# Performance work log

Measured on AMD Instinct MI355X. Metric: run time of the kernel, lower is better.

Reference implementation:

```python
import jax, jax.numpy as jnp
import numpy as np

N_NODES = 100000


def gcn_conv(x, src, dst, norm, W, b, n_nodes):
    # PyG GCNConv: h = x @ W; out[i] = sum_{j->i} norm_ij * h[j]; out += b
    h = x @ W  # [N, F_out]
    msg = h[src] * norm[:, None]  # [E+N, F_out] gather + scale
    out = jax.ops.segment_sum(msg, dst, num_segments=n_nodes)
    return out + b


def setup_inputs() -> dict:
    key = jax.random.key(0)
    ks = jax.random.split(key, 5)
    n, e = N_NODES, 1600000
    d_in, d_h, d_out = 512, 128, 40
    x = jax.random.normal(ks[0], (n, d_in), dtype=jnp.float32)
    edge_index = jax.random.randint(ks[1], (2, e), 0, n, dtype=jnp.int64)
    # Glorot-ish scaled weights
    W1 = jax.random.normal(ks[2], (d_in, d_h), dtype=jnp.float32) * (1.0 / np.sqrt(d_in))
    b1 = jnp.zeros((d_h,), dtype=jnp.float32)
    W2 = jax.random.normal(ks[3], (d_h, d_out), dtype=jnp.float32) * (1.0 / np.sqrt(d_h))
    b2 = jnp.zeros((d_out,), dtype=jnp.float32)
    return {"x": x, "edge_index": edge_index, "W1": W1, "b1": b1, "W2": W2, "b2": b2}


def reference(x, edge_index, W1, b1, W2, b2):
    n = x.shape[0]
    # add self-loops (PyG default add_self_loops=True)
    loop = jnp.arange(n, dtype=edge_index.dtype)
    src = jnp.concatenate([edge_index[0], loop])
    dst = jnp.concatenate([edge_index[1], loop])
    # symmetric normalization: deg^-1/2[src] * deg^-1/2[dst]
    deg = jax.ops.segment_sum(jnp.ones_like(dst, dtype=x.dtype), dst, num_segments=n)
    dinv = jnp.where(deg > 0, jax.lax.rsqrt(jnp.maximum(deg, 1.0)), 0.0)
    norm = dinv[src] * dinv[dst]
    h = gcn_conv(x, src, dst, norm, W1, b1, n)
    h = jax.nn.relu(h)
    h = gcn_conv(h, src, dst, norm, W2, b2, n)
    return jax.nn.log_softmax(h, axis=1)
```

## Files before the change

kernel.cpp:

```cpp
#include <hip/hip_runtime.h>
#include <math.h>

#define NBSHIFT 7
#define CHUNK1 8192
#define CHUNK 2048
#define BCAP 4608

typedef __attribute__((ext_vector_type(8))) short short8;
typedef __attribute__((ext_vector_type(4))) float v4f;

__device__ __forceinline__ unsigned short f2bf(float f) {
    unsigned int u = __float_as_uint(f);
    u += 0x7FFFu + ((u >> 16) & 1u);
    return (unsigned short)(u >> 16);
}
__device__ __forceinline__ unsigned int packbf(float a, float b) {
    return (unsigned int)f2bf(a) | ((unsigned int)f2bf(b) << 16);
}
__device__ __forceinline__ void bf8_to_f32(uint4 v, float* f) {
    f[0] = __uint_as_float(v.x << 16); f[1] = __uint_as_float(v.x & 0xFFFF0000u);
    f[2] = __uint_as_float(v.y << 16); f[3] = __uint_as_float(v.y & 0xFFFF0000u);
    f[4] = __uint_as_float(v.z << 16); f[5] = __uint_as_float(v.z & 0xFFFF0000u);
    f[6] = __uint_as_float(v.w << 16); f[7] = __uint_as_float(v.w & 0xFFFF0000u);
}

__global__ __launch_bounds__(256) void binsize_kernel(const int* __restrict__ dst, int E,
                                                      int* __restrict__ binSizes, int nbins) {
    __shared__ int hist[1024];
    int tid = threadIdx.x;
    for (int i = tid; i < nbins; i += 256) hist[i] = 0;
    __syncthreads();
    int base = blockIdx.x * CHUNK1;
    int cnt = E - base; if (cnt > CHUNK1) cnt = CHUNK1;
    for (int i = tid; i < cnt; i += 256) atomicAdd(&hist[dst[base + i] >> NBSHIFT], 1);
    __syncthreads();
    for (int i = tid; i < nbins; i += 256)
        if (hist[i]) atomicAdd(&binSizes[i], hist[i]);
}

__global__ __launch_bounds__(256) void binscan_kernel(const int* __restrict__ binSizes,
                                                      int* __restrict__ bin_base,
                                                      int* __restrict__ bin_cursor,
                                                      int nbins, int E,
                                                      int* __restrict__ offsets, int N) {
    __shared__ int vals[1024];
    __shared__ int ws[256];
    int tid = threadIdx.x;
    for (int i = tid; i < 1024; i += 256) vals[i] = (i < nbins) ? binSizes[i] : 0;
    __syncthreads();
    int s0 = vals[4 * tid];
    int s1 = s0 + vals[4 * tid + 1];
    int s2 = s1 + vals[4 * tid + 2];
    int s3 = s2 + vals[4 * tid + 3];
    ws[tid] = s3;
    __syncthreads();
    for (int off = 1; off < 256; off <<= 1) {
        int v = (tid >= off) ? ws[tid - off] : 0;
        __syncthreads();
        ws[tid] += v;
        __syncthreads();
    }
    int add = (tid > 0) ? ws[tid - 1] : 0;
    int i0 = 4 * tid;
    int b0 = add, b1 = add + s0, b2 = add + s1, b3 = add + s2;
    if (i0     < nbins) { bin_base[i0]     = b0; bin_cursor[i0]     = b0; }
    if (i0 + 1 < nbins) { bin_base[i0 + 1] = b1; bin_cursor[i0 + 1] = b1; }
    if (i0 + 2 < nbins) { bin_base[i0 + 2] = b2; bin_cursor[i0 + 2] = b2; }
    if (i0 + 3 < nbins) { bin_base[i0 + 3] = b3; bin_cursor[i0 + 3] = b3; }
    if (tid == 0) { bin_base[nbins] = E; offsets[N] = E; }
}

__global__ __launch_bounds__(256) void binpass_kernel(const int* __restrict__ src,
                                                      const int* __restrict__ dst, int E,
                                                      int* __restrict__ bin_cursor,
                                                      unsigned int* __restrict__ bpairs, int nbins) {
    __shared__ unsigned int pk[CHUNK];
    __shared__ unsigned short binOf[CHUNK];
    __shared__ int hist[1024];
    __shared__ int scanned[1024];
    __shared__ int wsum[256];
    __shared__ int rank_[1024];
    __shared__ int gbase[1024];
    int tid = threadIdx.x;
    int base = blockIdx.x * CHUNK;
    int cnt = E - base; if (cnt > CHUNK) cnt = CHUNK;

    for (int i = tid; i < 1024; i += 256) { hist[i] = 0; rank_[i] = 0; }
    __syncthreads();
    for (int i = tid; i < cnt; i += 256)
        atomicAdd(&hist[dst[base + i] >> NBSHIFT], 1);
    __syncthreads();
    int s0 = hist[4 * tid];
    int s1 = s0 + hist[4 * tid + 1];
    int s2 = s1 + hist[4 * tid + 2];
    int s3 = s2 + hist[4 * tid + 3];
    wsum[tid] = s3;
    __syncthreads();
    for (int off = 1; off < 256; off <<= 1) {
        int v = (tid >= off) ? wsum[tid - off] : 0;
        __syncthreads();
        wsum[tid] += v;
        __syncthreads();
    }
    int add = (tid > 0) ? wsum[tid - 1] : 0;
    scanned[4 * tid]     = add + s0;
    scanned[4 * tid + 1] = add + s1;
    scanned[4 * tid + 2] = add + s2;
    scanned[4 * tid + 3] = add + s3;
    __syncthreads();
    for (int i = tid; i < cnt; i += 256) {
        int d = dst[base + i];
        int s = src[base + i];
        int b = d >> NBSHIFT;
        unsigned int p = (unsigned int)s | ((unsigned int)(d & 127) << 17);
        int r = atomicAdd(&rank_[b], 1);
        int pos = scanned[b] - hist[b] + r;
        pk[pos] = p;
        binOf[pos] = (unsigned short)b;
    }
    __syncthreads();
    for (int b = tid; b < nbins; b += 256)
        if (hist[b] > 0) gbase[b] = atomicAdd(&bin_cursor[b], hist[b]);
    __syncthreads();
    for (int i = tid; i < cnt; i += 256) {
        int b = binOf[i];
        int local = i - (scanned[b] - hist[b]);
        bpairs[gbase[b] + local] = pk[i];
    }
}

__global__ __launch_bounds__(256) void binsort_kernel(const unsigned int* __restrict__ bpairs,
                                                      const int* __restrict__ bin_base,
                                                      int* __restrict__ ssrc,
                                                      int* __restrict__ offsets,
                                                      float* __restrict__ dinv, int N) {
    __shared__ unsigned int pin[BCAP];
    __shared__ int pout[BCAP];
    __shared__ int hist[128];
    __shared__ int pref[128];
    __shared__ int rank_[128];
    int b = blockIdx.x, tid = threadIdx.x;
    int start = bin_base[b], end = bin_base[b + 1];
    int cnt = end - start;
    if (cnt > BCAP) cnt = BCAP;
    int n0 = b << NBSHIFT;
    if (tid < 128) { hist[tid] = 0; rank_[tid] = 0; }
    __syncthreads();
    for (int i = tid; i < cnt; i += 256) {
        unsigned int p = bpairs[start + i];
        pin[i] = p;
        atomicAdd(&hist[p >> 17], 1);
    }
    __syncthreads();
    if (tid < 128) pref[tid] = hist[tid];
    __syncthreads();
    for (int off = 1; off < 128; off <<= 1) {
        int v = 0;
        if (tid < 128 && tid >= off) v = pref[tid - off];
        __syncthreads();
        if (tid < 128) pref[tid] += v;
        __syncthreads();
    }
    int node = n0 + tid;
    if (tid < 128 && node < N) {
        offsets[node] = start + pref[tid] - hist[tid];
        dinv[node] = rsqrtf((float)(hist[tid] + 1));
    }
    __syncthreads();
    for (int i = tid; i < cnt; i += 256) {
        unsigned int p = pin[i];
        int d = p >> 17;
        int r = atomicAdd(&rank_[d], 1);
        pout[pref[d] - hist[d] + r] = (int)(p & 0x1FFFFu);
    }
    __syncthreads();
    for (int i = tid; i < cnt; i += 256) ssrc[start + i] = pout[i];
}

__global__ void w1cast_kernel(const float* __restrict__ W1, unsigned short* __restrict__ W1s) {
    int idx = blockIdx.x * 256 + threadIdx.x;
    int k = idx >> 7, n = idx & 127;
    int dstIdx = ((k >> 6) << 13) | (n << 6) | ((((k >> 3) & 7) ^ (n & 7)) << 3) | (k & 7);
    W1s[dstIdx] = f2bf(W1[idx]);
}

#define BM1 128
#define BK1 64

__global__ __launch_bounds__(256) void gemm1_mfma_kernel(const float* __restrict__ X,
                                                         const unsigned short* __restrict__ W1s,
                                                         unsigned short* __restrict__ H, int N) {
    __shared__ unsigned short SMEM[16384];
    unsigned short* As = SMEM;
    unsigned short* Bs = SMEM + 8192;
    int tid = threadIdx.x;
    int wave = tid >> 6, lane = tid & 63;
    int quad = lane >> 4, lr = lane & 15;
    int mBase = (wave & 1) * 64, nBase = (wave >> 1) * 64;
    int rowBase = blockIdx.x * BM1;

    v4f zero4 = {0.f, 0.f, 0.f, 0.f};
    v4f acc[4][4];
    #pragma unroll
    for (int i = 0; i < 4; i++)
        #pragma unroll
        for (int j = 0; j < 4; j++) acc[i][j] = zero4;

    float4 pfA0[4], pfA1[4];
    uint4  pfB[4];

    #define LOAD_A(K0)                                                                  \
        _Pragma("unroll")                                                               \
        for (int t = 0; t < 4; t++) {                                                   \
            int idx = tid + t * 256;                                                    \
            int r = idx >> 3, c = idx & 7;                                              \
            int gr = rowBase + r;                                                       \
            const float4* p = (const float4*)(X + (size_t)gr * 512 + (K0) + c * 8);     \
            bool ok = gr < N;                                                           \
            pfA0[t] = ok ? p[0] : make_float4(0.f, 0.f, 0.f, 0.f);                      \
            pfA1[t] = ok ? p[1] : make_float4(0.f, 0.f, 0.f, 0.f);                      \
        }
    #define LOAD_B(K0)                                                                  \
        _Pragma("unroll")                                                               \
        for (int t = 0; t < 4; t++)                                                     \
            pfB[t] = *(const uint4*)(W1s + (((K0) >> 6) << 13) + ((tid + t * 256) << 3));

    LOAD_A(0); LOAD_B(0);

    for (int k0 = 0; k0 < 512; k0 += BK1) {
        __syncthreads();
        #pragma unroll
        for (int t = 0; t < 4; t++) {
            int idx = tid + t * 256;
            int r = idx >> 3, c = idx & 7;
            uint4 v;
            v.x = packbf(pfA0[t].x, pfA0[t].y); v.y = packbf(pfA0[t].z, pfA0[t].w);
            v.z = packbf(pfA1[t].x, pfA1[t].y); v.w = packbf(pfA1[t].z, pfA1[t].w);
            *(uint4*)(&As[(r << 6) + ((c ^ (r & 7)) << 3)]) = v;
        }
        #pragma unroll
        for (int t = 0; t < 4; t++)
            *(uint4*)(&Bs[(tid + t * 256) << 3]) = pfB[t];
        __syncthreads();
        if (k0 + BK1 < 512) { LOAD_A(k0 + BK1); LOAD_B(k0 + BK1); }
        #pragma unroll
        for (int kc = 0; kc < BK1; kc += 32) {
            int cb = kc >> 3;
            short8 aF[4], bF[4];
            #pragma unroll
            for (int i = 0; i < 4; i++) {
                int m = mBase + i * 16 + lr;
                aF[i] = *(const short8*)(&As[m * 64 + (((cb + quad) ^ (m & 7)) << 3)]);
            }
            #pragma unroll
            for (int j = 0; j < 4; j++) {
                int n = nBase + j * 16 + lr;
                bF[j] = *(const short8*)(&Bs[n * 64 + (((cb + quad) ^ (n & 7)) << 3)]);
            }
            #pragma unroll
            for (int i = 0; i < 4; i++)
                #pragma unroll
                for (int j = 0; j < 4; j++)
                    acc[i][j] = __builtin_amdgcn_mfma_f32_16x16x32_bf16(aF[i], bF[j], acc[i][j], 0, 0, 0);
        }
    }
    __syncthreads();
    unsigned short* Cs = SMEM;
    #pragma unroll
    for (int i = 0; i < 4; i++) {
        #pragma unroll
        for (int r = 0; r < 4; r++) {
            int m = mBase + i * 16 + quad * 4 + r;
            #pragma unroll
            for (int j = 0; j < 4; j++)
                Cs[m * 128 + ((nBase + j * 16 + lr) ^ ((m & 7) << 4))] = f2bf(acc[i][j][r]);
        }
    }
    __syncthreads();
    #pragma unroll
    for (int t = 0; t < 8; t++) {
        int idx = tid + t * 256;
        int row = idx >> 4, c = idx & 15;
        int gr = rowBase + row;
        if (gr < N)
            *(uint4*)(H + (size_t)gr * 128 + c * 8) =
                *(const uint4*)(&Cs[row * 128 + ((c * 8) ^ ((row & 7) << 4))]);
    }
    #undef LOAD_A
    #undef LOAD_B
}

__global__ __launch_bounds__(256) void agg1_kernel(const unsigned short* __restrict__ h1,
                                                   const int* __restrict__ offsets,
                                                   const int* __restrict__ ssrc,
                                                   const float* __restrict__ dinv,
                                                   const float* __restrict__ bias,
                                                   unsigned short* __restrict__ a1, int N) {
    int lane = threadIdx.x & 15;
    int node = (blockIdx.x << 4) + (threadIdx.x >> 4);
    if (node >= N) return;
    const uint4* h = (const uint4*)h1;
    float di = dinv[node];
    float acc[8], t[8];
    bf8_to_f32(h[(size_t)node * 16 + lane], t);
    #pragma unroll
    for (int i = 0; i < 8; i++) acc[i] = di * t[i];
    int e = offsets[node], e1 = offsets[node + 1];
    for (; e + 3 < e1; e += 4) {
        int sA = ssrc[e], sB = ssrc[e + 1], sC = ssrc[e + 2], sD = ssrc[e + 3];
        float wA = dinv[sA], wB = dinv[sB], wC = dinv[sC], wD = dinv[sD];
        uint4 vA = h[(size_t)sA * 16 + lane];
        uint4 vB = h[(size_t)sB * 16 + lane];
        uint4 vC = h[(size_t)sC * 16 + lane];
        uint4 vD = h[(size_t)sD * 16 + lane];
        float fA[8], fB[8], fC[8], fD[8];
        bf8_to_f32(vA, fA); bf8_to_f32(vB, fB); bf8_to_f32(vC, fC); bf8_to_f32(vD, fD);
        #pragma unroll
        for (int i = 0; i < 8; i++) {
            acc[i] = fmaf(wA, fA[i], acc[i]);
            acc[i] = fmaf(wB, fB[i], acc[i]);
            acc[i] = fmaf(wC, fC[i], acc[i]);
            acc[i] = fmaf(wD, fD[i], acc[i]);
        }
    }
    for (; e < e1; e++) {
        int s = ssrc[e];
        float w = dinv[s];
        float fs[8];
        bf8_to_f32(h[(size_t)s * 16 + lane], fs);
        #pragma unroll
        for (int i = 0; i < 8; i++) acc[i] = fmaf(w, fs[i], acc[i]);
    }
    float4 b0 = ((const float4*)bias)[lane * 2];
    float4 b1v = ((const float4*)bias)[lane * 2 + 1];
    float bb[8] = {b0.x, b0.y, b0.z, b0.w, b1v.x, b1v.y, b1v.z, b1v.w};
    float o[8];
    #pragma unroll
    for (int i = 0; i < 8; i++) o[i] = fmaxf(fmaf(di, acc[i], bb[i]), 0.f);
    uint4 pv;
    pv.x = packbf(o[0], o[1]); pv.y = packbf(o[2], o[3]);
    pv.z = packbf(o[4], o[5]); pv.w = packbf(o[6], o[7]);
    ((uint4*)a1)[(size_t)node * 16 + lane] = pv;
}

__global__ __launch_bounds__(256) void gemm2_kernel(const unsigned short* __restrict__ A,
                                                    const float* __restrict__ W,
                                                    float* __restrict__ H, int N) {
    __shared__ float As2[128][64];
    __shared__ float Ws[128 * 40];
    int tid = threadIdx.x;
    int rowBase = blockIdx.x * 64;

    #pragma unroll
    for (int l = 0; l < 4; l++) {
        int e = tid + l * 256;
        int r = e >> 4;
        int kk = (e & 15) << 3;
        int grow = rowBase + r;
        float f[8] = {0.f, 0.f, 0.f, 0.f, 0.f, 0.f, 0.f, 0.f};
        if (grow < N) {
            uint4 v = *(const uint4*)(A + (size_t)grow * 128 + kk);
            bf8_to_f32(v, f);
        }
        #pragma unroll
        for (int q = 0; q < 8; q++) As2[kk + q][r] = f[q];
    }
    #pragma unroll
    for (int l = 0; l < 5; l++) {
        int e = tid + l * 256;
        *(float4*)&Ws[e << 2] = *(const float4*)&W[e << 2];
    }
    __syncthreads();

    int tx = tid & 7;
    int ty = tid >> 3;
    float acc[2][5];
    #pragma unroll
    for (int r = 0; r < 2; r++)
        #pragma unroll
        for (int c = 0; c < 5; c++) acc[r][c] = 0.f;

    #pragma unroll 8
    for (int k = 0; k < 128; k++) {
        float a0 = As2[k][ty * 2];
        float a1v = As2[k][ty * 2 + 1];
        #pragma unroll
        for (int c = 0; c < 5; c++) {
            float w = Ws[k * 40 + tx * 5 + c];
            acc[0][c] = fmaf(a0, w, acc[0][c]);
            acc[1][c] = fmaf(a1v, w, acc[1][c]);
        }
    }
    #pragma unroll
    for (int r = 0; r < 2; r++) {
        int grow = rowBase + ty * 2 + r;
        if (grow < N) {
            #pragma unroll
            for (int c = 0; c < 5; c++) H[grow * 40 + tx * 5 + c] = acc[r][c];
        }
    }
}

__global__ __launch_bounds__(256) void agg2_kernel(const float* __restrict__ h2,
                                                   const int* __restrict__ offsets,
                                                   const int* __restrict__ ssrc,
                                                   const float* __restrict__ dinv,
                                                   const float* __restrict__ bias,
                                                   float* __restrict__ out, int N) {
    int lane = threadIdx.x & 15;
    int node = (blockIdx.x << 4) + (threadIdx.x >> 4);
    if (node >= N) return;
    const float4* h = (const float4*)h2;
    float di = dinv[node];
    bool act = lane < 10;
    float a0 = 0.f, a1 = 0.f, a2 = 0.f, a3 = 0.f;
    if (act) {
        float4 v = h[(size_t)node * 10 + lane];
        a0 = di * v.x; a1 = di * v.y; a2 = di * v.z; a3 = di * v.w;
    }
    int e = offsets[node], e1 = offsets[node + 1];
    for (; e + 3 < e1; e += 4) {
        int sA = ssrc[e], sB = ssrc[e + 1], sC = ssrc[e + 2], sD = ssrc[e + 3];
        float wA = dinv[sA], wB = dinv[sB], wC = dinv[sC], wD = dinv[sD];
        if (act) {
            float4 vA = h[(size_t)sA * 10 + lane];
            float4 vB = h[(size_t)sB * 10 + lane];
            float4 vC = h[(size_t)sC * 10 + lane];
            float4 vD = h[(size_t)sD * 10 + lane];
            a0 = fmaf(wA, vA.x, a0); a1 = fmaf(wA, vA.y, a1);
            a2 = fmaf(wA, vA.z, a2); a3 = fmaf(wA, vA.w, a3);
            a0 = fmaf(wB, vB.x, a0); a1 = fmaf(wB, vB.y, a1);
            a2 = fmaf(wB, vB.z, a2); a3 = fmaf(wB, vB.w, a3);
            a0 = fmaf(wC, vC.x, a0); a1 = fmaf(wC, vC.y, a1);
            a2 = fmaf(wC, vC.z, a2); a3 = fmaf(wC, vC.w, a3);
            a0 = fmaf(wD, vD.x, a0); a1 = fmaf(wD, vD.y, a1);
            a2 = fmaf(wD, vD.z, a2); a3 = fmaf(wD, vD.w, a3);
        }
    }
    for (; e < e1; e++) {
        int s = ssrc[e];
        float w = dinv[s];
        if (act) {
            float4 v = h[(size_t)s * 10 + lane];
            a0 = fmaf(w, v.x, a0); a1 = fmaf(w, v.y, a1);
            a2 = fmaf(w, v.z, a2); a3 = fmaf(w, v.w, a3);
        }
    }
    float v0 = -INFINITY, v1 = -INFINITY, v2 = -INFINITY, v3 = -INFINITY;
    if (act) {
        float4 bb = ((const float4*)bias)[lane];
        v0 = fmaf(di, a0, bb.x); v1 = fmaf(di, a1, bb.y);
        v2 = fmaf(di, a2, bb.z); v3 = fmaf(di, a3, bb.w);
    }
    float m = fmaxf(fmaxf(v0, v1), fmaxf(v2, v3));
    #pragma unroll
    for (int off = 8; off; off >>= 1) m = fmaxf(m, __shfl_xor(m, off, 16));
    float s = act ? (expf(v0 - m) + expf(v1 - m) + expf(v2 - m) + expf(v3 - m)) : 0.f;
    #pragma unroll
    for (int off = 8; off; off >>= 1) s += __shfl_xor(s, off, 16);
    if (act) {
        float ls = logf(s);
        float4 o;
        o.x = v0 - m - ls; o.y = v1 - m - ls; o.z = v2 - m - ls; o.w = v3 - m - ls;
        ((float4*)out)[(size_t)node * 10 + lane] = o;
    }
}

extern "C" void kernel_launch(void* const* d_in, const int* in_sizes, int n_in,
                              void* d_out, int out_size, void* d_ws, size_t ws_size,
                              hipStream_t stream) {
    const float* x  = (const float*)d_in[0];
    const int*   ei = (const int*)d_in[1];
    const float* W1 = (const float*)d_in[2];
    const float* b1 = (const float*)d_in[3];
    const float* W2 = (const float*)d_in[4];
    const float* b2 = (const float*)d_in[5];
    float* out = (float*)d_out;

    int N = in_sizes[0] / 512;
    int E = in_sizes[1] / 2;
    const int* src = ei;
    const int* dst = ei + E;
    int nbins = (N + 127) >> NBSHIFT;

    char* ws = (char*)d_ws;
    size_t off = 0;
    auto alloc = [&](size_t bytes) -> void* {
        void* p = ws + off;
        off += (bytes + 255) & ~(size_t)255;
        return p;
    };
    int*   offsets   = (int*)alloc((size_t)(N + 1) * 4);
    float* dinv      = (float*)alloc((size_t)N * 4);
    int*   binSizes  = (int*)alloc((size_t)nbins * 4);
    int*   bin_base  = (int*)alloc((size_t)(nbins + 1) * 4);
    int*   bin_cur   = (int*)alloc((size_t)nbins * 4);
    int*   ssrc      = (int*)alloc((size_t)E * 4);
    unsigned short* W1s = (unsigned short*)alloc((size_t)128 * 512 * 2);
    unsigned short* h1  = (unsigned short*)alloc((size_t)N * 128 * 2);
    unsigned short* a1  = (unsigned short*)alloc((size_t)N * 128 * 2);
    float* h2        = (float*)alloc((size_t)N * 40 * 4);
    unsigned int* bpairs = (unsigned int*)h1;
    (void)ws_size; (void)n_in; (void)out_size;

    hipMemsetAsync(binSizes, 0, (size_t)nbins * 4, stream);
    binsize_kernel<<<(E + CHUNK1 - 1) / CHUNK1, 256, 0, stream>>>(dst, E, binSizes, nbins);
    binscan_kernel<<<1, 256, 0, stream>>>(binSizes, bin_base, bin_cur, nbins, E, offsets, N);
    binpass_kernel<<<(E + CHUNK - 1) / CHUNK, 256, 0, stream>>>(src, dst, E, bin_cur, bpairs, nbins);
    binsort_kernel<<<nbins, 256, 0, stream>>>(bpairs, bin_base, ssrc, offsets, dinv, N);
    w1cast_kernel<<<256, 256, 0, stream>>>(W1, W1s);
    gemm1_mfma_kernel<<<(N + BM1 - 1) / BM1, 256, 0, stream>>>(x, W1s, h1, N);
    agg1_kernel<<<(N + 15) / 16, 256, 0, stream>>>(h1, offsets, ssrc, dinv, b1, a1, N);
    gemm2_kernel<<<(N + 63) / 64, 256, 0, stream>>>(a1, W2, h2, N);
    agg2_kernel<<<(N + 15) / 16, 256, 0, stream>>>(h2, offsets, ssrc, dinv, b2, out, N);
}
```

Measured before the change: 537.4 us.

## Prescale GEMM outputs by dinv and widen bins to 256 nodes

Each layer's GEMM epilogue now multiplies its output row by the source node's deg^-1/2. The two aggregation kernels can then sum neighbour features directly, without a random dinv[src] load and a multiply for every edge. The CSR build also switches to 256-node bins with 8192-edge chunks in the bin pass, which reduces global atomics and the number of bins. The trade-off is fewer binpass blocks, more LDS per block, and a slightly different rounding order because values are scaled before the bf16 cast.

```diff
diff --git a/kernel.cpp b/kernel.cpp
--- a/kernel.cpp
+++ b/kernel.cpp
@@ -1,10 +1,10 @@
 #include <hip/hip_runtime.h>
 #include <math.h>
 
-#define NBSHIFT 7
+#define NBSHIFT 8
 #define CHUNK1 8192
-#define CHUNK 2048
-#define BCAP 4608
+#define CHUNK 8192
+#define BCAP 4864
 
 typedef __attribute__((ext_vector_type(8))) short short8;
 typedef __attribute__((ext_vector_type(4))) float v4f;
@@ -26,9 +26,9 @@
 
 __global__ __launch_bounds__(256) void binsize_kernel(const int* __restrict__ dst, int E,
                                                       int* __restrict__ binSizes, int nbins) {
-    __shared__ int hist[1024];
+    __shared__ int hist[512];
     int tid = threadIdx.x;
-    for (int i = tid; i < nbins; i += 256) hist[i] = 0;
+    for (int i = tid; i < 512; i += 256) hist[i] = 0;
     __syncthreads();
     int base = blockIdx.x * CHUNK1;
     int cnt = E - base; if (cnt > CHUNK1) cnt = CHUNK1;
@@ -43,16 +43,14 @@
                                                       int* __restrict__ bin_cursor,
                                                       int nbins, int E,
                                                       int* __restrict__ offsets, int N) {
-    __shared__ int vals[1024];
+    __shared__ int vals[512];
     __shared__ int ws[256];
     int tid = threadIdx.x;
-    for (int i = tid; i < 1024; i += 256) vals[i] = (i < nbins) ? binSizes[i] : 0;
-    __syncthreads();
-    int s0 = vals[4 * tid];
-    int s1 = s0 + vals[4 * tid + 1];
-    int s2 = s1 + vals[4 * tid + 2];
-    int s3 = s2 + vals[4 * tid + 3];
-    ws[tid] = s3;
+    for (int i = tid; i < 512; i += 256) vals[i] = (i < nbins) ? binSizes[i] : 0;
+    __syncthreads();
+    int s0 = vals[2 * tid];
+    int s1 = s0 + vals[2 * tid + 1];
+    ws[tid] = s1;
     __syncthreads();
     for (int off = 1; off < 256; off <<= 1) {
         int v = (tid >= off) ? ws[tid - off] : 0;
@@ -61,12 +59,9 @@
         __syncthreads();
     }
     int add = (tid > 0) ? ws[tid - 1] : 0;
-    int i0 = 4 * tid;
-    int b0 = add, b1 = add + s0, b2 = add + s1, b3 = add + s2;
-    if (i0     < nbins) { bin_base[i0]     = b0; bin_cursor[i0]     = b0; }
-    if (i0 + 1 < nbins) { bin_base[i0 + 1] = b1; bin_cursor[i0 + 1] = b1; }
-    if (i0 + 2 < nbins) { bin_base[i0 + 2] = b2; bin_cursor[i0 + 2] = b2; }
-    if (i0 + 3 < nbins) { bin_base[i0 + 3] = b3; bin_cursor[i0 + 3] = b3; }
+    int i0 = 2 * tid;
+    if (i0     < nbins) { bin_base[i0]     = add;      bin_cursor[i0]     = add; }
+    if (i0 + 1 < nbins) { bin_base[i0 + 1] = add + s0; bin_cursor[i0 + 1] = add + s0; }
     if (tid == 0) { bin_base[nbins] = E; offsets[N] = E; }
 }
 
@@ -76,43 +71,34 @@
                                                       unsigned int* __restrict__ bpairs, int nbins) {
     __shared__ unsigned int pk[CHUNK];
     __shared__ unsigned short binOf[CHUNK];
-    __shared__ int hist[1024];
-    __shared__ int scanned[1024];
-    __shared__ int wsum[256];
-    __shared__ int rank_[1024];
-    __shared__ int gbase[1024];
+    __shared__ int hist[512];
+    __shared__ int scanned[512];
+    __shared__ int rank_[512];
+    __shared__ int gbase[512];
     int tid = threadIdx.x;
     int base = blockIdx.x * CHUNK;
     int cnt = E - base; if (cnt > CHUNK) cnt = CHUNK;
 
-    for (int i = tid; i < 1024; i += 256) { hist[i] = 0; rank_[i] = 0; }
+    for (int i = tid; i < 512; i += 256) { hist[i] = 0; rank_[i] = 0; }
     __syncthreads();
     for (int i = tid; i < cnt; i += 256)
         atomicAdd(&hist[dst[base + i] >> NBSHIFT], 1);
     __syncthreads();
-    int s0 = hist[4 * tid];
-    int s1 = s0 + hist[4 * tid + 1];
-    int s2 = s1 + hist[4 * tid + 2];
-    int s3 = s2 + hist[4 * tid + 3];
-    wsum[tid] = s3;
-    __syncthreads();
-    for (int off = 1; off < 256; off <<= 1) {
-        int v = (tid >= off) ? wsum[tid - off] : 0;
-        __syncthreads();
-        wsum[tid] += v;
-        __syncthreads();
-    }
-    int add = (tid > 0) ? wsum[tid - 1] : 0;
-    scanned[4 * tid]     = add + s0;
-    scanned[4 * tid + 1] = add + s1;
-    scanned[4 * tid + 2] = add + s2;
-    scanned[4 * tid + 3] = add + s3;
-    __syncthreads();
+    scanned[tid] = hist[tid]; scanned[tid + 256] = hist[tid + 256];
+    __syncthreads();
+    for (int off = 1; off < 512; off <<= 1) {
+        int i0 = tid, i1 = tid + 256;
+        int v0 = (i0 >= off) ? scanned[i0 - off] : 0;
+        int v1 = (i1 >= off) ? scanned[i1 - off] : 0;
+        __syncthreads();
+        scanned[i0] += v0; scanned[i1] += v1;
+        __syncthreads();
+    }
     for (int i = tid; i < cnt; i += 256) {
         int d = dst[base + i];
         int s = src[base + i];
         int b = d >> NBSHIFT;
-        unsigned int p = (unsigned int)s | ((unsigned int)(d & 127) << 17);
+        unsigned int p = (unsigned int)s | ((unsigned int)(d & 255) << 17);
         int r = atomicAdd(&rank_[b], 1);
         int pos = scanned[b] - hist[b] + r;
         pk[pos] = p;
@@ -136,15 +122,15 @@
                                                       float* __restrict__ dinv, int N) {
     __shared__ unsigned int pin[BCAP];
     __shared__ int pout[BCAP];
-    __shared__ int hist[128];
-    __shared__ int pref[128];
-    __shared__ int rank_[128];
+    __shared__ int hist[256];
+    __shared__ int pref[256];
+    __shared__ int rank_[256];
     int b = blockIdx.x, tid = threadIdx.x;
     int start = bin_base[b], end = bin_base[b + 1];
     int cnt = end - start;
     if (cnt > BCAP) cnt = BCAP;
     int n0 = b << NBSHIFT;
-    if (tid < 128) { hist[tid] = 0; rank_[tid] = 0; }
+    hist[tid] = 0; rank_[tid] = 0;
     __syncthreads();
     for (int i = tid; i < cnt; i += 256) {
         unsigned int p = bpairs[start + i];
@@ -152,17 +138,16 @@
         atomicAdd(&hist[p >> 17], 1);
     }
     __syncthreads();
-    if (tid < 128) pref[tid] = hist[tid];
-    __syncthreads();
-    for (int off = 1; off < 128; off <<= 1) {
-        int v = 0;
-        if (tid < 128 && tid >= off) v = pref[tid - off];
-        __syncthreads();
-        if (tid < 128) pref[tid] += v;
+    pref[tid] = hist[tid];
+    __syncthreads();
+    for (int off = 1; off < 256; off <<= 1) {
+        int v = (tid >= off) ? pref[tid - off] : 0;
+        __syncthreads();
+        pref[tid] += v;
         __syncthreads();
     }
     int node = n0 + tid;
-    if (tid < 128 && node < N) {
+    if (node < N) {
         offsets[node] = start + pref[tid] - hist[tid];
         dinv[node] = rsqrtf((float)(hist[tid] + 1));
     }
@@ -189,6 +174,7 @@
 
 __global__ __launch_bounds__(256) void gemm1_mfma_kernel(const float* __restrict__ X,
                                                          const unsigned short* __restrict__ W1s,
+                                                         const float* __restrict__ dinv,
                                                          unsigned short* __restrict__ H, int N) {
     __shared__ unsigned short SMEM[16384];
     unsigned short* As = SMEM;
@@ -271,9 +257,11 @@
         #pragma unroll
         for (int r = 0; r < 4; r++) {
             int m = mBase + i * 16 + quad * 4 + r;
+            int gr = rowBase + m;
+            float dv = (gr < N) ? dinv[gr] : 0.f;
             #pragma unroll
             for (int j = 0; j < 4; j++)
-                Cs[m * 128 + ((nBase + j * 16 + lr) ^ ((m & 7) << 4))] = f2bf(acc[i][j][r]);
+                Cs[m * 128 + ((nBase + j * 16 + lr) ^ ((m & 7) << 4))] = f2bf(dv * acc[i][j][r]);
         }
     }
     __syncthreads();
@@ -301,14 +289,11 @@
     if (node >= N) return;
     const uint4* h = (const uint4*)h1;
     float di = dinv[node];
-    float acc[8], t[8];
-    bf8_to_f32(h[(size_t)node * 16 + lane], t);
-    #pragma unroll
-    for (int i = 0; i < 8; i++) acc[i] = di * t[i];
+    float acc[8];
+    bf8_to_f32(h[(size_t)node * 16 + lane], acc);
     int e = offsets[node], e1 = offsets[node + 1];
     for (; e + 3 < e1; e += 4) {
         int sA = ssrc[e], sB = ssrc[e + 1], sC = ssrc[e + 2], sD = ssrc[e + 3];
-        float wA = dinv[sA], wB = dinv[sB], wC = dinv[sC], wD = dinv[sD];
         uint4 vA = h[(size_t)sA * 16 + lane];
         uint4 vB = h[(size_t)sB * 16 + lane];
         uint4 vC = h[(size_t)sC * 16 + lane];
@@ -316,20 +301,15 @@
         float fA[8], fB[8], fC[8], fD[8];
         bf8_to_f32(vA, fA); bf8_to_f32(vB, fB); bf8_to_f32(vC, fC); bf8_to_f32(vD, fD);
         #pragma unroll
-        for (int i = 0; i < 8; i++) {
-            acc[i] = fmaf(wA, fA[i], acc[i]);
-            acc[i] = fmaf(wB, fB[i], acc[i]);
-            acc[i] = fmaf(wC, fC[i], acc[i]);
-            acc[i] = fmaf(wD, fD[i], acc[i]);
-        }
+        for (int i = 0; i < 8; i++)
+            acc[i] += (fA[i] + fB[i]) + (fC[i] + fD[i]);
     }
     for (; e < e1; e++) {
         int s = ssrc[e];
-        float w = dinv[s];
         float fs[8];
         bf8_to_f32(h[(size_t)s * 16 + lane], fs);
         #pragma unroll
-        for (int i = 0; i < 8; i++) acc[i] = fmaf(w, fs[i], acc[i]);
+        for (int i = 0; i < 8; i++) acc[i] += fs[i];
     }
     float4 b0 = ((const float4*)bias)[lane * 2];
     float4 b1v = ((const float4*)bias)[lane * 2 + 1];
@@ -345,6 +325,7 @@
 
 __global__ __launch_bounds__(256) void gemm2_kernel(const unsigned short* __restrict__ A,
                                                     const float* __restrict__ W,
+                                                    const float* __restrict__ dinv,
                                                     float* __restrict__ H, int N) {
     __shared__ float As2[128][64];
     __shared__ float Ws[128 * 40];
@@ -395,8 +376,9 @@
     for (int r = 0; r < 2; r++) {
         int grow = rowBase + ty * 2 + r;
         if (grow < N) {
+            float dv = dinv[grow];
             #pragma unroll
-            for (int c = 0; c < 5; c++) H[grow * 40 + tx * 5 + c] = acc[r][c];
+            for (int c = 0; c < 5; c++) H[grow * 40 + tx * 5 + c] = dv * acc[r][c];
         }
     }
 }
@@ -416,34 +398,27 @@
     float a0 = 0.f, a1 = 0.f, a2 = 0.f, a3 = 0.f;
     if (act) {
         float4 v = h[(size_t)node * 10 + lane];
-        a0 = di * v.x; a1 = di * v.y; a2 = di * v.z; a3 = di * v.w;
+        a0 = v.x; a1 = v.y; a2 = v.z; a3 = v.w;
     }
     int e = offsets[node], e1 = offsets[node + 1];
     for (; e + 3 < e1; e += 4) {
         int sA = ssrc[e], sB = ssrc[e + 1], sC = ssrc[e + 2], sD = ssrc[e + 3];
-        float wA = dinv[sA], wB = dinv[sB], wC = dinv[sC], wD = dinv[sD];
         if (act) {
             float4 vA = h[(size_t)sA * 10 + lane];
             float4 vB = h[(size_t)sB * 10 + lane];
             float4 vC = h[(size_t)sC * 10 + lane];
             float4 vD = h[(size_t)sD * 10 + lane];
-            a0 = fmaf(wA, vA.x, a0); a1 = fmaf(wA, vA.y, a1);
-            a2 = fmaf(wA, vA.z, a2); a3 = fmaf(wA, vA.w, a3);
-            a0 = fmaf(wB, vB.x, a0); a1 = fmaf(wB, vB.y, a1);
-            a2 = fmaf(wB, vB.z, a2); a3 = fmaf(wB, vB.w, a3);
-            a0 = fmaf(wC, vC.x, a0); a1 = fmaf(wC, vC.y, a1);
-            a2 = fmaf(wC, vC.z, a2); a3 = fmaf(wC, vC.w, a3);
-            a0 = fmaf(wD, vD.x, a0); a1 = fmaf(wD, vD.y, a1);
-            a2 = fmaf(wD, vD.z, a2); a3 = fmaf(wD, vD.w, a3);
+            a0 += (vA.x + vB.x) + (vC.x + vD.x);
+            a1 += (vA.y + vB.y) + (vC.y + vD.y);
+            a2 += (vA.z + vB.z) + (vC.z + vD.z);
+            a3 += (vA.w + vB.w) + (vC.w + vD.w);
         }
     }
     for (; e < e1; e++) {
         int s = ssrc[e];
-        float w = dinv[s];
         if (act) {
             float4 v = h[(size_t)s * 10 + lane];
-            a0 = fmaf(w, v.x, a0); a1 = fmaf(w, v.y, a1);
-            a2 = fmaf(w, v.z, a2); a3 = fmaf(w, v.w, a3);
+            a0 += v.x; a1 += v.y; a2 += v.z; a3 += v.w;
         }
     }
     float v0 = -INFINITY, v1 = -INFINITY, v2 = -INFINITY, v3 = -INFINITY;
@@ -481,7 +456,7 @@
     int E = in_sizes[1] / 2;
     const int* src = ei;
     const int* dst = ei + E;
-    int nbins = (N + 127) >> NBSHIFT;
+    int nbins = (N + 255) >> NBSHIFT;
 
     char* ws = (char*)d_ws;
     size_t off = 0;
@@ -509,8 +484,8 @@
     binpass_kernel<<<(E + CHUNK - 1) / CHUNK, 256, 0, stream>>>(src, dst, E, bin_cur, bpairs, nbins);
     binsort_kernel<<<nbins, 256, 0, stream>>>(bpairs, bin_base, ssrc, offsets, dinv, N);
     w1cast_kernel<<<256, 256, 0, stream>>>(W1, W1s);
-    gemm1_mfma_kernel<<<(N + BM1 - 1) / BM1, 256, 0, stream>>>(x, W1s, h1, N);
+    gemm1_mfma_kernel<<<(N + BM1 - 1) / BM1, 256, 0, stream>>>(x, W1s, dinv, h1, N);
     agg1_kernel<<<(N + 15) / 16, 256, 0, stream>>>(h1, offsets, ssrc, dinv, b1, a1, N);
-    gemm2_kernel<<<(N + 63) / 64, 256, 0, stream>>>(a1, W2, h2, N);
+    gemm2_kernel<<<(N + 63) / 64, 256, 0, stream>>>(a1, W2, dinv, h2, N);
     agg2_kernel<<<(N + 15) / 16, 256, 0, stream>>>(h2, offsets, ssrc, dinv, b2, out, N);
 }
```

New measurement: 529.5 us. About the same (-1.5%).
